# Performance work log

Measured on AMD Instinct MI355X. Metric: run time of the kernel, lower is better.

## Reference

```python
import jax, jax.numpy as jnp
import numpy as np

N_NODES = 100000
N_EDGES = 1200000
D = 64
E_CHARGE = np.float32(1.602176634e-19)   # elementary charge (fp32, like the torch buffer)
EPS0 = np.float32(8.8541878128e-12)      # vacuum permittivity (fp32 buffer)


def _mish(x):
    return x * jnp.tanh(jax.nn.softplus(x))


def _mlp(x, w1, b1, w2, b2):
    # nn.Linear convention: y = x @ W.T + b
    h = _mish(x @ w1.T + b1)
    return h @ w2.T + b2


def setup_inputs() -> dict:
    key = jax.random.key(0)
    ks = jax.random.split(key, 20)
    s = 1.0 / np.sqrt(D)
    inp = {
        "node_feats": jax.random.normal(ks[0], (N_NODES, D), jnp.float32),
        "edge_feats": jax.random.normal(ks[1], (N_EDGES, D), jnp.float32),
        "src": jax.random.randint(ks[2], (N_EDGES,), 0, N_NODES),
        "dst": jax.random.randint(ks[3], (N_EDGES,), 0, N_NODES),
    }
    names = ["ws", "wd", "we", "wm"]
    i = 4
    for nm in names:
        inp[nm + "_w1"] = jax.random.normal(ks[i], (D, D), jnp.float32) * s; i += 1
        inp[nm + "_b1"] = jax.random.normal(ks[i], (D,), jnp.float32) * s; i += 1
        inp[nm + "_w2"] = jax.random.normal(ks[i], (D, D), jnp.float32) * s; i += 1
        inp[nm + "_b2"] = jax.random.normal(ks[i], (D,), jnp.float32) * s; i += 1
    return inp


def reference(node_feats, edge_feats, src, dst,
              ws_w1, ws_b1, ws_w2, ws_b2,
              wd_w1, wd_b1, wd_w2, wd_b2,
              we_w1, we_b1, we_w2, we_b2,
              wm_w1, wm_b1, wm_w2, wm_b2):
    # node MLPs then per-edge gather
    h_src = _mlp(node_feats, ws_w1, ws_b1, ws_w2, ws_b2)[src]   # [E, D]
    h_dst = _mlp(node_feats, wd_w1, wd_b1, wd_w2, wd_b2)[dst]   # [E, D]
    ef = _mlp(edge_feats, we_w1, we_b1, we_w2, we_b2)            # [E, D]
    # h_nodes * e^2 / (4*pi*eps0 * edge * 1e-10), all in fp32 like torch
    num = h_src * h_dst * (E_CHARGE ** 2)
    den = np.float32(4.0 * np.pi) * EPS0 * ef * np.float32(1e-10)
    h_nodes = num / den                                          # [E, D]
    m = _mlp(h_nodes, wm_w1, wm_b1, wm_w2, wm_b2)                # [E, D]
    # scatter-sum messages into destination nodes
    h = jax.ops.segment_sum(m, dst, num_segments=N_NODES)        # [N, D]
    return jax.nn.softplus(node_feats + h)
```

## Files before the change

### kernel.cpp

```cpp
#include <hip/hip_runtime.h>
#include <math.h>

#define NNODES 100000
#define NEDGES 1200000

#define C_EC   1.602176634e-19f
#define C_E2   (C_EC * C_EC)
#define C_4PI  12.566370614359172f
#define C_EPS0 8.8541878128e-12f
#define C_A    (C_4PI * C_EPS0)
#define C_B    1e-10f

typedef __attribute__((ext_vector_type(8))) short bf16x8;
typedef __attribute__((ext_vector_type(4))) float f32x4;
typedef __attribute__((ext_vector_type(4))) unsigned short u16x4;

__device__ __forceinline__ void wave_sync() {
    __builtin_amdgcn_fence(__ATOMIC_ACQ_REL, "wavefront");
    __builtin_amdgcn_wave_barrier();
}

__device__ __forceinline__ unsigned short f2bf(float f) {
    unsigned u = __float_as_uint(f);
    u += 0x7fffu + ((u >> 16) & 1u);
    return (unsigned short)(u >> 16);
}
__device__ __forceinline__ float bf2f(unsigned short s) {
    return __uint_as_float(((unsigned)s) << 16);
}
__device__ __forceinline__ float softplus_f(float x) {
    return fmaxf(x, 0.0f) + log1pf(__expf(-fabsf(x)));
}
__device__ __forceinline__ float mish_f(float x) {
    float e = __expf(fminf(x, 30.0f));
    float n = e * e + 2.0f * e;
    return x * n * __builtin_amdgcn_rcpf(n + 2.0f);
}


__device__ __forceinline__ void mfma_layer(const unsigned short* xs,
                                           const unsigned short* __restrict__ wg,
                                           const float* __restrict__ bias,
                                           int lane, f32x4 acc[4])
{
    const int l15 = lane & 15, q = lane >> 4;
    bf16x8 a0 = *(const bf16x8*)(xs + l15 * 72 + q * 8);
    bf16x8 a1 = *(const bf16x8*)(xs + l15 * 72 + 32 + q * 8);
    #pragma unroll
    for (int t = 0; t < 4; ++t) {
        float bv = bias[t * 16 + l15];
        acc[t] = (f32x4){bv, bv, bv, bv};
        bf16x8 b0 = *(const bf16x8*)(wg + (t * 16 + l15) * 64 + q * 8);
        bf16x8 b1 = *(const bf16x8*)(wg + (t * 16 + l15) * 64 + 32 + q * 8);
        acc[t] = __builtin_amdgcn_mfma_f32_16x16x32_bf16(a0, b0, acc[t], 0, 0, 0);
        acc[t] = __builtin_amdgcn_mfma_f32_16x16x32_bf16(a1, b1, acc[t], 0, 0, 0);
    }
}

__device__ __forceinline__ void mish_to_lds_perm(const f32x4 acc[4], unsigned short* hid, int lane)
{
    const int l15 = lane & 15, q = lane >> 4;
    #pragma unroll
    for (int j = 0; j < 4; ++j) {
        u16x4 v;
        v[0] = f2bf(mish_f(acc[0][j]));
        v[1] = f2bf(mish_f(acc[1][j]));
        v[2] = f2bf(mish_f(acc[2][j]));
        v[3] = f2bf(mish_f(acc[3][j]));
        *(u16x4*)(hid + (q * 4 + j) * 72 + l15 * 4) = v;
    }
}

__global__ __launch_bounds__(256) void convert_w_kernel(
    const float* __restrict__ w0, const float* __restrict__ w1,
    const float* __restrict__ w2, const float* __restrict__ w3,
    const float* __restrict__ w4, const float* __restrict__ w5,
    const float* __restrict__ w6, const float* __restrict__ w7,
    unsigned short* __restrict__ wbf)
{
    int g = blockIdx.x * 256 + threadIdx.x;
    int m = g >> 10;
    int e = (g & 1023) * 4;
    const float* w;
    switch (m) {
        case 0: w = w0; break; case 1: w = w1; break;
        case 2: w = w2; break; case 3: w = w3; break;
        case 4: w = w4; break; case 5: w = w5; break;
        case 6: w = w6; break; default: w = w7; break;
    }
    float4 v = *(const float4*)(w + e);
    int n = e >> 6, k = e & 63;
    bool perm = (m == 1) || (m == 3) || (m >= 5);
    int kk = perm ? ((k & 15) * 4 + (k >> 4)) : k;
    int st = perm ? 4 : 1;
    unsigned short* dp = wbf + m * 4096 + n * 64 + kk;
    dp[0] = f2bf(v.x); dp[st] = f2bf(v.y); dp[2 * st] = f2bf(v.z); dp[3 * st] = f2bf(v.w);
}

__global__ __launch_bounds__(256) void node_mlp_kernel(
    const float* __restrict__ x,
    const unsigned short* __restrict__ wbf,
    const float* __restrict__ bs1, const float* __restrict__ bs2,
    const float* __restrict__ bd1, const float* __restrict__ bd2,
    unsigned short* __restrict__ hs, unsigned short* __restrict__ hd,
    float* __restrict__ out)
{
    __shared__ __align__(16) unsigned short xs[64 * 72];
    __shared__ __align__(16) unsigned short hid[64 * 72];
    const int t = threadIdx.x, lane = t & 63, wave = t >> 6;
    const int row0 = blockIdx.x * 64 + wave * 16;
    unsigned short* xw = xs + wave * 16 * 72;
    unsigned short* hw = hid + wave * 16 * 72;
    const int l15 = lane & 15, q = lane >> 4;

    {
        int r = lane >> 2, c4 = lane & 3;
        if (row0 + r < NNODES) {
            float4 z = make_float4(0.f, 0.f, 0.f, 0.f);
            #pragma unroll
            for (int i = 0; i < 4; ++i)
                *(float4*)(out + (size_t)(row0 + r) * 64 + (c4 + i * 4) * 4) = z;
        }
    }

    {
        int r = lane >> 2, c4 = lane & 3;
        #pragma unroll
        for (int i = 0; i < 4; ++i) {
            int col = (c4 + i * 4) * 4;
            float4 v = make_float4(0.f, 0.f, 0.f, 0.f);
            if (row0 + r < NNODES) v = *(const float4*)(x + (size_t)(row0 + r) * 64 + col);
            unsigned short* dp = xw + r * 72 + col;
            dp[0] = f2bf(v.x); dp[1] = f2bf(v.y); dp[2] = f2bf(v.z); dp[3] = f2bf(v.w);
        }
    }
    wave_sync();

    f32x4 acc[4];
    mfma_layer(xw, wbf + 0 * 4096, bs1, lane, acc);
    wave_sync();
    mish_to_lds_perm(acc, hw, lane);
    wave_sync();
    mfma_layer(hw, wbf + 1 * 4096, bs2, lane, acc);
    #pragma unroll
    for (int j = 0; j < 4; ++j) {
        int row = row0 + q * 4 + j;
        if (row < NNODES) {
            u16x4 v;
            v[0] = f2bf(acc[0][j]); v[1] = f2bf(acc[1][j]);
            v[2] = f2bf(acc[2][j]); v[3] = f2bf(acc[3][j]);
            *(u16x4*)(hs + (size_t)row * 64 + l15 * 4) = v;
        }
    }
    mfma_layer(xw, wbf + 2 * 4096, bd1, lane, acc);
    wave_sync();
    mish_to_lds_perm(acc, hw, lane);
    wave_sync();
    mfma_layer(hw, wbf + 3 * 4096, bd2, lane, acc);
    #pragma unroll
    for (int j = 0; j < 4; ++j) {
        int row = row0 + q * 4 + j;
        if (row < NNODES) {
            u16x4 v;
            v[0] = f2bf(acc[0][j]); v[1] = f2bf(acc[1][j]);
            v[2] = f2bf(acc[2][j]); v[3] = f2bf(acc[3][j]);
            *(u16x4*)(hd + (size_t)row * 64 + l15 * 4) = v;
        }
    }
}

__global__ __launch_bounds__(256) void edge_kernel(
    const float* __restrict__ efeat,
    const unsigned short* __restrict__ hs, const unsigned short* __restrict__ hd,
    const int* __restrict__ src, const int* __restrict__ dst,
    const unsigned short* __restrict__ wbf,
    const float* __restrict__ be1, const float* __restrict__ be2,
    const float* __restrict__ bm1, const float* __restrict__ bm2,
    float* __restrict__ out)
{
    __shared__ __align__(16) unsigned short xs[64 * 72];
    __shared__ __align__(16) unsigned short hid[64 * 72];
    const int t = threadIdx.x, lane = t & 63, wave = t >> 6;
    const int e0 = blockIdx.x * 64 + wave * 16;
    unsigned short* xw = xs + wave * 16 * 72;
    unsigned short* hw = hid + wave * 16 * 72;
    const int l15 = lane & 15, q = lane >> 4;

    {
        int r = lane >> 2, c4 = lane & 3;
        #pragma unroll
        for (int i = 0; i < 4; ++i) {
            int col = (c4 + i * 4) * 4;
            float4 v = *(const float4*)(efeat + (size_t)(e0 + r) * 64 + col);
            unsigned short* dp = xw + r * 72 + col;
            dp[0] = f2bf(v.x); dp[1] = f2bf(v.y); dp[2] = f2bf(v.z); dp[3] = f2bf(v.w);
        }
    }
    int sj[4], dj[4];
    #pragma unroll
    for (int j = 0; j < 4; ++j) {
        sj[j] = src[e0 + q * 4 + j];
        dj[j] = dst[e0 + q * 4 + j];
    }
    u16x4 va[4], vb[4];
    #pragma unroll
    for (int j = 0; j < 4; ++j) {
        va[j] = *(const u16x4*)(hs + (size_t)sj[j] * 64 + l15 * 4);
        vb[j] = *(const u16x4*)(hd + (size_t)dj[j] * 64 + l15 * 4);
    }
    wave_sync();

    f32x4 acc[4], ef[4];
    mfma_layer(xw, wbf + 4 * 4096, be1, lane, acc);
    wave_sync();
    mish_to_lds_perm(acc, hw, lane);
    wave_sync();
    mfma_layer(hw, wbf + 5 * 4096, be2, lane, ef);
    wave_sync();

    #pragma unroll
    for (int j = 0; j < 4; ++j) {
        u16x4 hv;
        #pragma unroll
        for (int t4 = 0; t4 < 4; ++t4) {
            float a = bf2f(va[j][t4]);
            float b = bf2f(vb[j][t4]);
            float den = (C_A * ef[t4][j]) * C_B;
            float num = (a * b) * C_E2;
            float h = (den != 0.0f) ? num * __builtin_amdgcn_rcpf(den) : 0.0f;
            h = fminf(fmaxf(h, -1e30f), 1e30f);
            hv[t4] = f2bf(h);
        }
        *(u16x4*)(xw + (q * 4 + j) * 72 + l15 * 4) = hv;
    }
    wave_sync();

    mfma_layer(xw, wbf + 6 * 4096, bm1, lane, acc);
    wave_sync();
    mish_to_lds_perm(acc, hw, lane);
    wave_sync();
    mfma_layer(hw, wbf + 7 * 4096, bm2, lane, acc);

    #pragma unroll
    for (int j = 0; j < 4; ++j) {
        float* p = out + (size_t)dj[j] * 64;
        #pragma unroll
        for (int t4 = 0; t4 < 4; ++t4)
            atomicAdd(p + t4 * 16 + l15, acc[t4][j]);
    }
}

__global__ __launch_bounds__(256) void finalize_kernel(
    const float* __restrict__ nf, float* __restrict__ out)
{
    int g = blockIdx.x * 256 + threadIdx.x;
    float4 a = ((const float4*)nf)[g];
    float4 h = ((float4*)out)[g];
    float4 o;
    o.x = softplus_f(a.x + h.x);
    o.y = softplus_f(a.y + h.y);
    o.z = softplus_f(a.z + h.z);
    o.w = softplus_f(a.w + h.w);
    ((float4*)out)[g] = o;
}

extern "C" void kernel_launch(void* const* d_in, const int* in_sizes, int n_in,
                              void* d_out, int out_size, void* d_ws, size_t ws_size,
                              hipStream_t stream)
{
    const float* node_feats = (const float*)d_in[0];
    const float* edge_feats = (const float*)d_in[1];
    const int*   src        = (const int*)d_in[2];
    const int*   dst        = (const int*)d_in[3];
    const float* ws_w1 = (const float*)d_in[4];
    const float* ws_b1 = (const float*)d_in[5];
    const float* ws_w2 = (const float*)d_in[6];
    const float* ws_b2 = (const float*)d_in[7];
    const float* wd_w1 = (const float*)d_in[8];
    const float* wd_b1 = (const float*)d_in[9];
    const float* wd_w2 = (const float*)d_in[10];
    const float* wd_b2 = (const float*)d_in[11];
    const float* we_w1 = (const float*)d_in[12];
    const float* we_b1 = (const float*)d_in[13];
    const float* we_w2 = (const float*)d_in[14];
    const float* we_b2 = (const float*)d_in[15];
    const float* wm_w1 = (const float*)d_in[16];
    const float* wm_b1 = (const float*)d_in[17];
    const float* wm_w2 = (const float*)d_in[18];
    const float* wm_b2 = (const float*)d_in[19];

    unsigned short* wbf = (unsigned short*)d_ws;
    unsigned short* hs  = wbf + 8 * 4096;
    unsigned short* hd  = hs + (size_t)NNODES * 64;

    convert_w_kernel<<<32, 256, 0, stream>>>(
        ws_w1, ws_w2, wd_w1, wd_w2, we_w1, we_w2, wm_w1, wm_w2, wbf);

    node_mlp_kernel<<<(NNODES + 63) / 64, 256, 0, stream>>>(
        node_feats, wbf, ws_b1, ws_b2, wd_b1, wd_b2, hs, hd, (float*)d_out);

    edge_kernel<<<NEDGES / 64, 256, 0, stream>>>(
        edge_feats, hs, hd, src, dst, wbf, we_b1, we_b2, wm_b1, wm_b2, (float*)d_out);

    finalize_kernel<<<(NNODES * 64) / (256 * 4), 256, 0, stream>>>(
        node_feats, (float*)d_out);
}
```

Before: 781.9 us.

## Persist edge waves over multiple tiles with register prefetch and direct A-fragment loads

Each edge-kernel wave now handles five 16-edge tiles in sequence and prefetches the next tile's edge features, indices and gathered node rows into registers while the current tile's MLP and atomics run. Input features are loaded straight into the MFMA A-operand layout in registers, so the LDS staging buffer and its syncs are gone. Biases are hoisted into registers once per wave. This hides gather latency and cuts LDS traffic, at the cost of higher register pressure (launch bounds set to 4) and fewer blocks.

```diff
diff --git a/kernel.cpp b/kernel.cpp
--- a/kernel.cpp
+++ b/kernel.cpp
@@ -3,6 +3,7 @@
 
 #define NNODES 100000
 #define NEDGES 1200000
+#define TPB_E  5
 
 #define C_EC   1.602176634e-19f
 #define C_E2   (C_EC * C_EC)
@@ -37,24 +38,37 @@
     return x * n * __builtin_amdgcn_rcpf(n + 2.0f);
 }
 
-
-__device__ __forceinline__ void mfma_layer(const unsigned short* xs,
-                                           const unsigned short* __restrict__ wg,
-                                           const float* __restrict__ bias,
-                                           int lane, f32x4 acc[4])
-{
-    const int l15 = lane & 15, q = lane >> 4;
-    bf16x8 a0 = *(const bf16x8*)(xs + l15 * 72 + q * 8);
-    bf16x8 a1 = *(const bf16x8*)(xs + l15 * 72 + 32 + q * 8);
+__device__ __forceinline__ bf16x8 pack_bf16(float4 a, float4 b) {
+    bf16x8 r;
+    r[0] = f2bf(a.x); r[1] = f2bf(a.y); r[2] = f2bf(a.z); r[3] = f2bf(a.w);
+    r[4] = f2bf(b.x); r[5] = f2bf(b.y); r[6] = f2bf(b.z); r[7] = f2bf(b.w);
+    return r;
+}
+
+
+__device__ __forceinline__ void mfma_regs(bf16x8 a0, bf16x8 a1,
+                                          const unsigned short* __restrict__ wg,
+                                          const float bv[4], int l15, int q,
+                                          f32x4 acc[4])
+{
     #pragma unroll
     for (int t = 0; t < 4; ++t) {
-        float bv = bias[t * 16 + l15];
-        acc[t] = (f32x4){bv, bv, bv, bv};
+        acc[t] = (f32x4){bv[t], bv[t], bv[t], bv[t]};
         bf16x8 b0 = *(const bf16x8*)(wg + (t * 16 + l15) * 64 + q * 8);
         bf16x8 b1 = *(const bf16x8*)(wg + (t * 16 + l15) * 64 + 32 + q * 8);
         acc[t] = __builtin_amdgcn_mfma_f32_16x16x32_bf16(a0, b0, acc[t], 0, 0, 0);
         acc[t] = __builtin_amdgcn_mfma_f32_16x16x32_bf16(a1, b1, acc[t], 0, 0, 0);
     }
+}
+
+__device__ __forceinline__ void mfma_lds(const unsigned short* hw,
+                                         const unsigned short* __restrict__ wg,
+                                         const float bv[4], int l15, int q,
+                                         f32x4 acc[4])
+{
+    bf16x8 a0 = *(const bf16x8*)(hw + l15 * 72 + q * 8);
+    bf16x8 a1 = *(const bf16x8*)(hw + l15 * 72 + 32 + q * 8);
+    mfma_regs(a0, a1, wg, bv, l15, q, acc);
 }
 
 __device__ __forceinline__ void mish_to_lds_perm(const f32x4 acc[4], unsigned short* hid, int lane)
@@ -105,11 +119,9 @@
     unsigned short* __restrict__ hs, unsigned short* __restrict__ hd,
     float* __restrict__ out)
 {
-    __shared__ __align__(16) unsigned short xs[64 * 72];
     __shared__ __align__(16) unsigned short hid[64 * 72];
     const int t = threadIdx.x, lane = t & 63, wave = t >> 6;
     const int row0 = blockIdx.x * 64 + wave * 16;
-    unsigned short* xw = xs + wave * 16 * 72;
     unsigned short* hw = hid + wave * 16 * 72;
     const int l15 = lane & 15, q = lane >> 4;
 
@@ -123,25 +135,33 @@
         }
     }
 
+    float4 v0 = make_float4(0.f,0.f,0.f,0.f), v1 = v0, v2 = v0, v3 = v0;
     {
-        int r = lane >> 2, c4 = lane & 3;
-        #pragma unroll
-        for (int i = 0; i < 4; ++i) {
-            int col = (c4 + i * 4) * 4;
-            float4 v = make_float4(0.f, 0.f, 0.f, 0.f);
-            if (row0 + r < NNODES) v = *(const float4*)(x + (size_t)(row0 + r) * 64 + col);
-            unsigned short* dp = xw + r * 72 + col;
-            dp[0] = f2bf(v.x); dp[1] = f2bf(v.y); dp[2] = f2bf(v.z); dp[3] = f2bf(v.w);
-        }
-    }
-    wave_sync();
+        int arow = row0 + l15;
+        if (arow < NNODES) {
+            const float* rp = x + (size_t)arow * 64 + q * 8;
+            v0 = *(const float4*)(rp);
+            v1 = *(const float4*)(rp + 4);
+            v2 = *(const float4*)(rp + 32);
+            v3 = *(const float4*)(rp + 36);
+        }
+    }
+    bf16x8 a0 = pack_bf16(v0, v1);
+    bf16x8 a1 = pack_bf16(v2, v3);
+
+    float bs1v[4], bs2v[4], bd1v[4], bd2v[4];
+    #pragma unroll
+    for (int i = 0; i < 4; ++i) {
+        bs1v[i] = bs1[i * 16 + l15]; bs2v[i] = bs2[i * 16 + l15];
+        bd1v[i] = bd1[i * 16 + l15]; bd2v[i] = bd2[i * 16 + l15];
+    }
 
     f32x4 acc[4];
-    mfma_layer(xw, wbf + 0 * 4096, bs1, lane, acc);
+    mfma_regs(a0, a1, wbf + 0 * 4096, bs1v, l15, q, acc);
     wave_sync();
     mish_to_lds_perm(acc, hw, lane);
     wave_sync();
-    mfma_layer(hw, wbf + 1 * 4096, bs2, lane, acc);
+    mfma_lds(hw, wbf + 1 * 4096, bs2v, l15, q, acc);
     #pragma unroll
     for (int j = 0; j < 4; ++j) {
         int row = row0 + q * 4 + j;
@@ -152,11 +172,11 @@
             *(u16x4*)(hs + (size_t)row * 64 + l15 * 4) = v;
         }
     }
-    mfma_layer(xw, wbf + 2 * 4096, bd1, lane, acc);
+    mfma_regs(a0, a1, wbf + 2 * 4096, bd1v, l15, q, acc);
     wave_sync();
     mish_to_lds_perm(acc, hw, lane);
     wave_sync();
-    mfma_layer(hw, wbf + 3 * 4096, bd2, lane, acc);
+    mfma_lds(hw, wbf + 3 * 4096, bd2v, l15, q, acc);
     #pragma unroll
     for (int j = 0; j < 4; ++j) {
         int row = row0 + q * 4 + j;
@@ -169,7 +189,30 @@
     }
 }
 
-__global__ __launch_bounds__(256) void edge_kernel(
+__device__ __forceinline__ void load_tile(
+    int e0, const float* __restrict__ efeat,
+    const int* __restrict__ src, const int* __restrict__ dst,
+    const unsigned short* __restrict__ hs, const unsigned short* __restrict__ hd,
+    int l15, int q,
+    float4 v[4], int4& sj, int4& dj, u16x4 va[4], u16x4 vb[4])
+{
+    const float* rp = efeat + (size_t)(e0 + l15) * 64 + q * 8;
+    v[0] = *(const float4*)(rp);
+    v[1] = *(const float4*)(rp + 4);
+    v[2] = *(const float4*)(rp + 32);
+    v[3] = *(const float4*)(rp + 36);
+    sj = *(const int4*)(src + e0 + q * 4);
+    dj = *(const int4*)(dst + e0 + q * 4);
+    const int sjj[4] = {sj.x, sj.y, sj.z, sj.w};
+    const int djj[4] = {dj.x, dj.y, dj.z, dj.w};
+    #pragma unroll
+    for (int j = 0; j < 4; ++j) {
+        va[j] = *(const u16x4*)(hs + (size_t)sjj[j] * 64 + l15 * 4);
+        vb[j] = *(const u16x4*)(hd + (size_t)djj[j] * 64 + l15 * 4);
+    }
+}
+
+__global__ __launch_bounds__(256, 4) void edge_kernel(
     const float* __restrict__ efeat,
     const unsigned short* __restrict__ hs, const unsigned short* __restrict__ hd,
     const int* __restrict__ src, const int* __restrict__ dst,
@@ -178,75 +221,77 @@
     const float* __restrict__ bm1, const float* __restrict__ bm2,
     float* __restrict__ out)
 {
-    __shared__ __align__(16) unsigned short xs[64 * 72];
     __shared__ __align__(16) unsigned short hid[64 * 72];
     const int t = threadIdx.x, lane = t & 63, wave = t >> 6;
-    const int e0 = blockIdx.x * 64 + wave * 16;
-    unsigned short* xw = xs + wave * 16 * 72;
     unsigned short* hw = hid + wave * 16 * 72;
     const int l15 = lane & 15, q = lane >> 4;
-
-    {
-        int r = lane >> 2, c4 = lane & 3;
+    const int base = blockIdx.x * (4 * TPB_E * 16) + wave * (TPB_E * 16);
+
+    float be1v[4], be2v[4], bm1v[4], bm2v[4];
+    #pragma unroll
+    for (int i = 0; i < 4; ++i) {
+        be1v[i] = be1[i * 16 + l15]; be2v[i] = be2[i * 16 + l15];
+        bm1v[i] = bm1[i * 16 + l15]; bm2v[i] = bm2[i * 16 + l15];
+    }
+
+    float4 v[4];  int4 sj, dj;  u16x4 va[4], vb[4];
+    float4 nv[4]; int4 nsj, ndj; u16x4 nva[4], nvb[4];
+    load_tile(base, efeat, src, dst, hs, hd, l15, q, v, sj, dj, va, vb);
+
+    #pragma unroll
+    for (int i = 0; i < TPB_E; ++i) {
+        bf16x8 a0 = pack_bf16(v[0], v[1]);
+        bf16x8 a1 = pack_bf16(v[2], v[3]);
+        f32x4 acc[4], ef[4];
+
+        mfma_regs(a0, a1, wbf + 4 * 4096, be1v, l15, q, acc);
+        wave_sync();
+        mish_to_lds_perm(acc, hw, lane);
+        wave_sync();
+        mfma_lds(hw, wbf + 5 * 4096, be2v, l15, q, ef);
+        wave_sync();
+
         #pragma unroll
-        for (int i = 0; i < 4; ++i) {
-            int col = (c4 + i * 4) * 4;
-            float4 v = *(const float4*)(efeat + (size_t)(e0 + r) * 64 + col);
-            unsigned short* dp = xw + r * 72 + col;
-            dp[0] = f2bf(v.x); dp[1] = f2bf(v.y); dp[2] = f2bf(v.z); dp[3] = f2bf(v.w);
-        }
-    }
-    int sj[4], dj[4];
-    #pragma unroll
-    for (int j = 0; j < 4; ++j) {
-        sj[j] = src[e0 + q * 4 + j];
-        dj[j] = dst[e0 + q * 4 + j];
-    }
-    u16x4 va[4], vb[4];
-    #pragma unroll
-    for (int j = 0; j < 4; ++j) {
-        va[j] = *(const u16x4*)(hs + (size_t)sj[j] * 64 + l15 * 4);
-        vb[j] = *(const u16x4*)(hd + (size_t)dj[j] * 64 + l15 * 4);
-    }
-    wave_sync();
-
-    f32x4 acc[4], ef[4];
-    mfma_layer(xw, wbf + 4 * 4096, be1, lane, acc);
-    wave_sync();
-    mish_to_lds_perm(acc, hw, lane);
-    wave_sync();
-    mfma_layer(hw, wbf + 5 * 4096, be2, lane, ef);
-    wave_sync();
-
-    #pragma unroll
-    for (int j = 0; j < 4; ++j) {
-        u16x4 hv;
+        for (int j = 0; j < 4; ++j) {
+            u16x4 hv;
+            #pragma unroll
+            for (int t4 = 0; t4 < 4; ++t4) {
+                float a = bf2f(va[j][t4]);
+                float b = bf2f(vb[j][t4]);
+                float den = (C_A * ef[t4][j]) * C_B;
+                float num = (a * b) * C_E2;
+                float h = (den != 0.0f) ? num * __builtin_amdgcn_rcpf(den) : 0.0f;
+                h = fminf(fmaxf(h, -1e30f), 1e30f);
+                hv[t4] = f2bf(h);
+            }
+            *(u16x4*)(hw + (q * 4 + j) * 72 + l15 * 4) = hv;
+        }
+        wave_sync();
+
+        mfma_lds(hw, wbf + 6 * 4096, bm1v, l15, q, acc);
+        wave_sync();
+        mish_to_lds_perm(acc, hw, lane);
+        wave_sync();
+        mfma_lds(hw, wbf + 7 * 4096, bm2v, l15, q, acc);
+
+        if (i + 1 < TPB_E)
+            load_tile(base + (i + 1) * 16, efeat, src, dst, hs, hd, l15, q,
+                      nv, nsj, ndj, nva, nvb);
+
+        const int djj[4] = {dj.x, dj.y, dj.z, dj.w};
         #pragma unroll
-        for (int t4 = 0; t4 < 4; ++t4) {
-            float a = bf2f(va[j][t4]);
-            float b = bf2f(vb[j][t4]);
-            float den = (C_A * ef[t4][j]) * C_B;
-            float num = (a * b) * C_E2;
-            float h = (den != 0.0f) ? num * __builtin_amdgcn_rcpf(den) : 0.0f;
-            h = fminf(fmaxf(h, -1e30f), 1e30f);
-            hv[t4] = f2bf(h);
-        }
-        *(u16x4*)(xw + (q * 4 + j) * 72 + l15 * 4) = hv;
-    }
-    wave_sync();
-
-    mfma_layer(xw, wbf + 6 * 4096, bm1, lane, acc);
-    wave_sync();
-    mish_to_lds_perm(acc, hw, lane);
-    wave_sync();
-    mfma_layer(hw, wbf + 7 * 4096, bm2, lane, acc);
-
-    #pragma unroll
-    for (int j = 0; j < 4; ++j) {
-        float* p = out + (size_t)dj[j] * 64;
-        #pragma unroll
-        for (int t4 = 0; t4 < 4; ++t4)
-            atomicAdd(p + t4 * 16 + l15, acc[t4][j]);
+        for (int j = 0; j < 4; ++j) {
+            float* p = out + (size_t)djj[j] * 64;
+            #pragma unroll
+            for (int t4 = 0; t4 < 4; ++t4)
+                atomicAdd(p + t4 * 16 + l15, acc[t4][j]);
+        }
+
+        if (i + 1 < TPB_E) {
+            #pragma unroll
+            for (int j = 0; j < 4; ++j) { v[j] = nv[j]; va[j] = nva[j]; vb[j] = nvb[j]; }
+            sj = nsj; dj = ndj;
+        }
     }
 }
 
@@ -299,7 +344,7 @@
     node_mlp_kernel<<<(NNODES + 63) / 64, 256, 0, stream>>>(
         node_feats, wbf, ws_b1, ws_b2, wd_b1, wd_b2, hs, hd, (float*)d_out);
 
-    edge_kernel<<<NEDGES / 64, 256, 0, stream>>>(
+    edge_kernel<<<NEDGES / (4 * TPB_E * 16), 256, 0, stream>>>(
         edge_feats, hs, hd, src, dst, wbf, we_b1, we_b2, wm_b1, wm_b2, (float*)d_out);
 
     finalize_kernel<<<(NNODES * 64) / (256 * 4), 256, 0, stream>>>(
```

Result: slower. 920.1 us (+17.7%).
